# Kernel tuning notes

Hardware: AMD Instinct MI355X
Metric: run time of the kernel (lower is better)

## Reference

```python
import jax, jax.numpy as jnp
import numpy as np

RADIUS = 0.2
NSAMPLE = 32


def ball_query(new_xyz, xyz, radius, nsample):
    # new_xyz: (B, M, 3), xyz: (B, N, 3) -> idx: (B, M, nsample) int32
    B, M, _ = new_xyz.shape
    N = xyz.shape[1]
    # pairwise squared distances (B, M, N)
    diff = new_xyz[:, :, None, :] - xyz[:, None, :, :]
    dist2 = jnp.sum(diff * diff, axis=-1)
    mask = dist2 < (radius * radius)
    ar = jnp.arange(N, dtype=jnp.int32)
    masked = jnp.where(mask, ar[None, None, :], jnp.int32(N + 1))  # (B,M,N)
    sorted_idx = jnp.sort(masked, axis=2)[:, :, :nsample]          # (B,M,nsample)
    invalid = sorted_idx >= N
    first = sorted_idx[:, :, 0:1]
    idx = jnp.where(invalid, jnp.broadcast_to(first, sorted_idx.shape), sorted_idx)
    return idx


def group_points(points, idx):
    # points: (B, C, N), idx: (B, M, nsample) -> (B, C, M, nsample)
    B, C, N = points.shape
    M, ns = idx.shape[1], idx.shape[2]
    flat = jnp.broadcast_to(idx.reshape(B, 1, M * ns), (B, C, M * ns))
    return jnp.take_along_axis(points, flat, axis=2).reshape(B, C, M, ns)


def setup_inputs() -> dict:
    key = jax.random.key(0)
    k1, k2, k3 = jax.random.split(key, 3)
    xyz = jax.random.uniform(k1, (8, 16384, 3), dtype=jnp.float32)
    new_xyz = jax.random.uniform(k2, (8, 1024, 3), dtype=jnp.float32)
    features = jax.random.normal(k3, (8, 64, 16384), dtype=jnp.float32)
    return {"xyz": xyz, "new_xyz": new_xyz, "features": features}


def reference(xyz, new_xyz, features):
    idx = ball_query(new_xyz, xyz, RADIUS, NSAMPLE)          # (B,M,ns)
    xyz_t = jnp.transpose(xyz, (0, 2, 1))                    # (B,3,N)
    grouped_xyz = group_points(xyz_t, idx)                   # (B,3,M,ns)
    grouped_xyz = grouped_xyz - jnp.transpose(new_xyz, (0, 2, 1))[:, :, :, None]
    grouped_features = group_points(features, idx)           # (B,C,M,ns)
    new_features = jnp.concatenate([grouped_xyz, grouped_features], axis=1)
    return new_features                                      # (B, 3+C, M, ns)
```

## Files before the change

### kernel.cpp

```cpp
#include <hip/hip_runtime.h>


#define N_PTS   16384
#define M_Q     1024
#define B_SZ    8
#define NSAMP   32
#define NCH     64
#define R2      0.04f
#define OUT_CH  (3 + NCH)

typedef float f4 __attribute__((ext_vector_type(4)));

__global__ __launch_bounds__(256) void transpose_kernel(
    const float* __restrict__ feat, float* __restrict__ ft)
{
    __shared__ float tile[64][65];
    const int b   = blockIdx.x & 7;
    const int n0  = (blockIdx.x >> 3) << 6;
    const int tid = threadIdx.x;
    const float* __restrict__ fb = feat + (size_t)b * NCH * N_PTS;
    float* __restrict__ tb       = ft   + ((size_t)b * N_PTS + n0) * NCH;

#pragma unroll
    for (int j = 0; j < 16; ++j) {
        const int idx = j * 256 + tid;
        const int c = idx >> 6, nn = idx & 63;
        tile[c][nn] = __builtin_nontemporal_load(&fb[(size_t)c * N_PTS + n0 + nn]);
    }
    __syncthreads();
    const int c4 = tid & 15;
    const int r  = tid >> 4;
#pragma unroll
    for (int j = 0; j < 4; ++j) {
        const int nn = j * 16 + r;
        f4 o;
        o.x = tile[c4 * 4 + 0][nn];
        o.y = tile[c4 * 4 + 1][nn];
        o.z = tile[c4 * 4 + 2][nn];
        o.w = tile[c4 * 4 + 3][nn];
        *(f4*)(&tb[(size_t)nn * NCH + c4 * 4]) = o;
    }
}

__global__ __launch_bounds__(256) void qg_main(
    const float* __restrict__ xyz,
    const float* __restrict__ new_xyz,
    const float* __restrict__ ft,
    float* __restrict__ out)
{
    const int tid  = threadIdx.x;
    const int w    = tid >> 6;
    const int lane = tid & 63;
    const int b    = blockIdx.x & 7;
    const int m    = ((blockIdx.x >> 3) << 2) + w;
    const int q    = (b << 10) + m;

    __shared__ float pxyz[4][NSAMP][4];
    __shared__ float tile[4][32][33];

    const float cx = new_xyz[q * 3 + 0];
    const float cy = new_xyz[q * 3 + 1];
    const float cz = new_xyz[q * 3 + 2];
    const float* __restrict__ xb = xyz + (size_t)b * N_PTS * 3;

    const unsigned long long lmask = (1ull << lane) - 1ull;
    int cnt = 0;
    float Ax = xb[lane * 3 + 0],        Ay = xb[lane * 3 + 1],        Az = xb[lane * 3 + 2];
    float Bx = xb[(64 + lane) * 3 + 0], By = xb[(64 + lane) * 3 + 1], Bz = xb[(64 + lane) * 3 + 2];

    for (int base = 0; ; base += 128) {
        const int  nbase = base + 128;
        const bool more  = nbase < N_PTS;
        const int  pA = more ? nbase + lane : lane;
        const int  pB = pA + 64;
        const float nAx = xb[pA * 3 + 0], nAy = xb[pA * 3 + 1], nAz = xb[pA * 3 + 2];
        const float nBx = xb[pB * 3 + 0], nBy = xb[pB * 3 + 1], nBz = xb[pB * 3 + 2];

        {
            const float dx = __fsub_rn(cx, Ax), dy = __fsub_rn(cy, Ay), dz = __fsub_rn(cz, Az);
            const float d2 = __fadd_rn(__fadd_rn(__fmul_rn(dx, dx), __fmul_rn(dy, dy)),
                                       __fmul_rn(dz, dz));
            const bool hit = d2 < R2;
            const unsigned long long mk = __ballot(hit);
            if (hit) {
                const int slot = cnt + __popcll(mk & lmask);
                if (slot < NSAMP) {
                    pxyz[w][slot][0] = Ax;
                    pxyz[w][slot][1] = Ay;
                    pxyz[w][slot][2] = Az;
                    pxyz[w][slot][3] = __int_as_float(base + lane);
                }
            }
            cnt += (int)__popcll(mk);
        }
        {
            const float dx = __fsub_rn(cx, Bx), dy = __fsub_rn(cy, By), dz = __fsub_rn(cz, Bz);
            const float d2 = __fadd_rn(__fadd_rn(__fmul_rn(dx, dx), __fmul_rn(dy, dy)),
                                       __fmul_rn(dz, dz));
            const bool hit = d2 < R2;
            const unsigned long long mk = __ballot(hit);
            if (hit) {
                const int slot = cnt + __popcll(mk & lmask);
                if (slot < NSAMP) {
                    pxyz[w][slot][0] = Bx;
                    pxyz[w][slot][1] = By;
                    pxyz[w][slot][2] = Bz;
                    pxyz[w][slot][3] = __int_as_float(base + 64 + lane);
                }
            }
            cnt += (int)__popcll(mk);
        }
        if (cnt >= NSAMP || !more) break;
        Ax = nAx; Ay = nAy; Az = nAz;
        Bx = nBx; By = nBy; Bz = nBz;
    }

    if (lane < NSAMP && cnt < NSAMP) {
        float v0x, v0y, v0z, v0w;
        if (cnt > 0) {
            v0x = pxyz[w][0][0]; v0y = pxyz[w][0][1];
            v0z = pxyz[w][0][2]; v0w = pxyz[w][0][3];
        } else {
            v0x = xb[0]; v0y = xb[1]; v0z = xb[2]; v0w = __int_as_float(0);
        }
        if (lane >= cnt) {
            pxyz[w][lane][0] = v0x; pxyz[w][lane][1] = v0y;
            pxyz[w][lane][2] = v0z; pxyz[w][lane][3] = v0w;
        }
    }

    float* __restrict__ ob = out + ((size_t)b * OUT_CH * M_Q + (size_t)m) * NSAMP;

    if (lane < 24) {
        const int c  = lane >> 3;
        const int s4 = lane & 7;
        const float ctr = (c == 0) ? cx : ((c == 1) ? cy : cz);
        f4 o;
        o.x = __fsub_rn(pxyz[w][s4 * 4 + 0][c], ctr);
        o.y = __fsub_rn(pxyz[w][s4 * 4 + 1][c], ctr);
        o.z = __fsub_rn(pxyz[w][s4 * 4 + 2][c], ctr);
        o.w = __fsub_rn(pxyz[w][s4 * 4 + 3][c], ctr);
        __builtin_nontemporal_store(o, (f4*)&ob[(size_t)c * (M_Q * NSAMP) + s4 * 4]);
    }

    const float* __restrict__ ftb = ft + (size_t)b * N_PTS * NCH;
    const int sgrp = lane >> 3;
    const int c4   = lane & 7;

#pragma unroll
    for (int chunk = 0; chunk < 2; ++chunk) {
        f4 vals[4];
#pragma unroll
        for (int i = 0; i < 4; ++i) {
            const int s = i * 8 + sgrp;
            const int n = __float_as_int(pxyz[w][s][3]);
            vals[i] = *(const f4*)(ftb + (size_t)n * NCH + chunk * 32 + c4 * 4);
        }
#pragma unroll
        for (int i = 0; i < 4; ++i) {
            const int s = i * 8 + sgrp;
            tile[w][c4 * 4 + 0][s] = vals[i].x;
            tile[w][c4 * 4 + 1][s] = vals[i].y;
            tile[w][c4 * 4 + 2][s] = vals[i].z;
            tile[w][c4 * 4 + 3][s] = vals[i].w;
        }
#pragma unroll
        for (int j = 0; j < 4; ++j) {
            const int c_loc = j * 8 + (lane >> 3);
            const int s4    = lane & 7;
            f4 o;
            o.x = tile[w][c_loc][s4 * 4 + 0];
            o.y = tile[w][c_loc][s4 * 4 + 1];
            o.z = tile[w][c_loc][s4 * 4 + 2];
            o.w = tile[w][c_loc][s4 * 4 + 3];
            __builtin_nontemporal_store(
                o, (f4*)&ob[(size_t)(3 + chunk * 32 + c_loc) * (M_Q * NSAMP) + s4 * 4]);
        }
    }
}

__global__ __launch_bounds__(256) void qg_fallback(
    const float* __restrict__ xyz, const float* __restrict__ new_xyz,
    const float* __restrict__ feat, float* __restrict__ out)
{
    const int tid  = threadIdx.x;
    const int w    = tid >> 6;
    const int lane = tid & 63;
    const int q    = blockIdx.x * 4 + w;
    const int b    = q >> 10;
    const int m    = q & (M_Q - 1);

    __shared__ int idx_sh[4][NSAMP];

    const float cx = new_xyz[q * 3 + 0];
    const float cy = new_xyz[q * 3 + 1];
    const float cz = new_xyz[q * 3 + 2];
    const float* __restrict__ xb = xyz + (size_t)b * N_PTS * 3;

    int cnt = 0;
    for (int base = 0; base < N_PTS && cnt < NSAMP; base += 64) {
        const int n = base + lane;
        const float dx = __fsub_rn(cx, xb[n * 3 + 0]);
        const float dy = __fsub_rn(cy, xb[n * 3 + 1]);
        const float dz = __fsub_rn(cz, xb[n * 3 + 2]);
        const float d2 = __fadd_rn(__fadd_rn(__fmul_rn(dx, dx), __fmul_rn(dy, dy)),
                                   __fmul_rn(dz, dz));
        const bool hit = d2 < R2;
        const unsigned long long mk = __ballot(hit);
        if (hit) {
            const int slot = cnt + __popcll(mk & ((1ull << lane) - 1ull));
            if (slot < NSAMP) idx_sh[w][slot] = n;
        }
        cnt += (int)__popcll(mk);
    }
    __syncthreads();
    if (lane < NSAMP) {
        const int v0 = (cnt > 0) ? idx_sh[w][0] : 0;
        if (lane >= cnt) idx_sh[w][lane] = v0;
    }
    __syncthreads();

    const float* __restrict__ fb = feat + (size_t)b * NCH * N_PTS;
    float* __restrict__ ob = out + ((size_t)b * OUT_CH * M_Q + (size_t)m) * NSAMP;
    for (int e = lane; e < OUT_CH * NSAMP; e += 64) {
        const int c = e >> 5, s = e & 31;
        const int n = idx_sh[w][s];
        float v;
        if (c < 3) {
            const float ctr = (c == 0) ? cx : ((c == 1) ? cy : cz);
            v = __fsub_rn(xb[n * 3 + c], ctr);
        } else {
            v = fb[(size_t)(c - 3) * N_PTS + n];
        }
        ob[(size_t)c * (M_Q * NSAMP) + s] = v;
    }
}

extern "C" void kernel_launch(void* const* d_in, const int* in_sizes, int n_in,
                              void* d_out, int out_size, void* d_ws, size_t ws_size,
                              hipStream_t stream) {
    const float* xyz     = (const float*)d_in[0];
    const float* new_xyz = (const float*)d_in[1];
    const float* feat    = (const float*)d_in[2];
    float* out           = (float*)d_out;

    const size_t need = (size_t)B_SZ * N_PTS * NCH * sizeof(float);
    if (ws_size >= need) {
        transpose_kernel<<<B_SZ * (N_PTS / 64), 256, 0, stream>>>(feat, (float*)d_ws);
        qg_main<<<(B_SZ * M_Q) / 4, 256, 0, stream>>>(xyz, new_xyz, (const float*)d_ws, out);
    } else {
        qg_fallback<<<(B_SZ * M_Q) / 4, 256, 0, stream>>>(xyz, new_xyz, feat, out);
    }
}
```

Measured before the change: 143.4 us.

## Split ball query into fused transpose kernel with SoA xyz and separate grouping

A new pass converts xyz to structure-of-arrays so the ball-query scan can use vectorized f4 loads over 256 points per iteration. The ball query now runs in the same launch as the feature transpose, with interleaved block types, so the latency-bound search overlaps the bandwidth-bound transpose. Relative offsets and indices are written to a workspace meta buffer that a separate group kernel reads. This adds a kernel launch and extra workspace traffic, and the scan drops the software prefetch of the next chunk.

Measured after the change: 125.9 us. -12.2%, faster.

```diff
diff --git a/kernel.cpp b/kernel.cpp
--- a/kernel.cpp
+++ b/kernel.cpp
@@ -11,40 +11,137 @@
 
 typedef float f4 __attribute__((ext_vector_type(4)));
 
-__global__ __launch_bounds__(256) void transpose_kernel(
-    const float* __restrict__ feat, float* __restrict__ ft)
+__global__ __launch_bounds__(256) void soa_kernel(
+    const float* __restrict__ xyz,
+    float* __restrict__ xs, float* __restrict__ ys, float* __restrict__ zs)
+{
+    const int i = blockIdx.x * 256 + threadIdx.x;
+    const float* src = xyz + (size_t)i * 3;
+    xs[i] = src[0];
+    ys[i] = src[1];
+    zs[i] = src[2];
+}
+
+__global__ __launch_bounds__(256) void fat_kernel(
+    const float* __restrict__ feat,
+    const float* __restrict__ new_xyz,
+    const float* __restrict__ xs, const float* __restrict__ ys,
+    const float* __restrict__ zs,
+    float* __restrict__ ft,
+    f4* __restrict__ meta)
 {
     __shared__ float tile[64][65];
-    const int b   = blockIdx.x & 7;
-    const int n0  = (blockIdx.x >> 3) << 6;
-    const int tid = threadIdx.x;
-    const float* __restrict__ fb = feat + (size_t)b * NCH * N_PTS;
-    float* __restrict__ tb       = ft   + ((size_t)b * N_PTS + n0) * NCH;
-
-#pragma unroll
-    for (int j = 0; j < 16; ++j) {
-        const int idx = j * 256 + tid;
-        const int c = idx >> 6, nn = idx & 63;
-        tile[c][nn] = __builtin_nontemporal_load(&fb[(size_t)c * N_PTS + n0 + nn]);
-    }
-    __syncthreads();
-    const int c4 = tid & 15;
-    const int r  = tid >> 4;
-#pragma unroll
-    for (int j = 0; j < 4; ++j) {
-        const int nn = j * 16 + r;
-        f4 o;
-        o.x = tile[c4 * 4 + 0][nn];
-        o.y = tile[c4 * 4 + 1][nn];
-        o.z = tile[c4 * 4 + 2][nn];
-        o.w = tile[c4 * 4 + 3][nn];
-        *(f4*)(&tb[(size_t)nn * NCH + c4 * 4]) = o;
-    }
-}
-
-__global__ __launch_bounds__(256) void qg_main(
-    const float* __restrict__ xyz,
-    const float* __restrict__ new_xyz,
+    __shared__ float pxyz[4][NSAMP][4];
+    const int tid  = threadIdx.x;
+    const int u    = (blockIdx.x & 7) | ((blockIdx.x >> 4) << 3);
+    const int type = (blockIdx.x >> 3) & 1;
+    const int b    = u & 7;
+
+    if (type == 0) {
+        const int n0 = (u >> 3) << 6;
+        const float* __restrict__ fb = feat + (size_t)b * NCH * N_PTS;
+        float* __restrict__ tb       = ft   + ((size_t)b * N_PTS + n0) * NCH;
+#pragma unroll
+        for (int j = 0; j < 16; ++j) {
+            const int idx = j * 256 + tid;
+            const int c = idx >> 6, nn = idx & 63;
+            tile[c][nn] = __builtin_nontemporal_load(&fb[(size_t)c * N_PTS + n0 + nn]);
+        }
+        __syncthreads();
+        const int c4 = tid & 15;
+        const int r  = tid >> 4;
+#pragma unroll
+        for (int j = 0; j < 4; ++j) {
+            const int nn = j * 16 + r;
+            f4 o;
+            o.x = tile[c4 * 4 + 0][nn];
+            o.y = tile[c4 * 4 + 1][nn];
+            o.z = tile[c4 * 4 + 2][nn];
+            o.w = tile[c4 * 4 + 3][nn];
+            *(f4*)(&tb[(size_t)nn * NCH + c4 * 4]) = o;
+        }
+        return;
+    }
+
+    const int w    = tid >> 6;
+    const int lane = tid & 63;
+    const int m    = ((u >> 3) << 2) + w;
+    const int q    = (b << 10) + m;
+
+    const float cx = new_xyz[q * 3 + 0];
+    const float cy = new_xyz[q * 3 + 1];
+    const float cz = new_xyz[q * 3 + 2];
+    const float* __restrict__ xsb = xs + (size_t)b * N_PTS;
+    const float* __restrict__ ysb = ys + (size_t)b * N_PTS;
+    const float* __restrict__ zsb = zs + (size_t)b * N_PTS;
+
+    const unsigned long long lt = (1ull << lane) - 1ull;
+    int cnt = 0;
+    for (int base = 0; base < N_PTS; base += 256) {
+        const int p0 = base + 4 * lane;
+        const f4 X = *(const f4*)(xsb + p0);
+        const f4 Y = *(const f4*)(ysb + p0);
+        const f4 Z = *(const f4*)(zsb + p0);
+        float dxs[4], dys[4], dzs[4];
+        unsigned long long bl[4];
+        bool hits[4];
+#pragma unroll
+        for (int j = 0; j < 4; ++j) {
+            const float dx = __fsub_rn(cx, X[j]);
+            const float dy = __fsub_rn(cy, Y[j]);
+            const float dz = __fsub_rn(cz, Z[j]);
+            const float d2 = __fadd_rn(__fadd_rn(__fmul_rn(dx, dx), __fmul_rn(dy, dy)),
+                                       __fmul_rn(dz, dz));
+            dxs[j] = dx; dys[j] = dy; dzs[j] = dz;
+            hits[j] = d2 < R2;
+            bl[j]   = __ballot(hits[j]);
+        }
+        const int pre = __popcll(bl[0] & lt) + __popcll(bl[1] & lt)
+                      + __popcll(bl[2] & lt) + __popcll(bl[3] & lt);
+        int own = 0;
+#pragma unroll
+        for (int j = 0; j < 4; ++j) {
+            if (hits[j]) {
+                const int slot = cnt + pre + own;
+                if (slot < NSAMP) {
+                    pxyz[w][slot][0] = -dxs[j];
+                    pxyz[w][slot][1] = -dys[j];
+                    pxyz[w][slot][2] = -dzs[j];
+                    pxyz[w][slot][3] = __int_as_float(p0 + j);
+                }
+            }
+            own += (int)((bl[j] >> lane) & 1ull);
+        }
+        cnt += __popcll(bl[0]) + __popcll(bl[1]) + __popcll(bl[2]) + __popcll(bl[3]);
+        if (cnt >= NSAMP) break;
+    }
+
+    if (lane < NSAMP && cnt < NSAMP) {
+        float v0x, v0y, v0z, v0w;
+        if (cnt > 0) {
+            v0x = pxyz[w][0][0]; v0y = pxyz[w][0][1];
+            v0z = pxyz[w][0][2]; v0w = pxyz[w][0][3];
+        } else {
+            v0x = __fsub_rn(xsb[0], cx); v0y = __fsub_rn(ysb[0], cy);
+            v0z = __fsub_rn(zsb[0], cz); v0w = __int_as_float(0);
+        }
+        if (lane >= cnt) {
+            pxyz[w][lane][0] = v0x; pxyz[w][lane][1] = v0y;
+            pxyz[w][lane][2] = v0z; pxyz[w][lane][3] = v0w;
+        }
+    }
+    if (lane < NSAMP) {
+        f4 mv;
+        mv.x = pxyz[w][lane][0];
+        mv.y = pxyz[w][lane][1];
+        mv.z = pxyz[w][lane][2];
+        mv.w = pxyz[w][lane][3];
+        meta[(size_t)q * NSAMP + lane] = mv;
+    }
+}
+
+__global__ __launch_bounds__(256) void group_kernel(
+    const f4* __restrict__ meta,
     const float* __restrict__ ft,
     float* __restrict__ out)
 {
@@ -58,75 +155,12 @@
     __shared__ float pxyz[4][NSAMP][4];
     __shared__ float tile[4][32][33];
 
-    const float cx = new_xyz[q * 3 + 0];
-    const float cy = new_xyz[q * 3 + 1];
-    const float cz = new_xyz[q * 3 + 2];
-    const float* __restrict__ xb = xyz + (size_t)b * N_PTS * 3;
-
-    const unsigned long long lmask = (1ull << lane) - 1ull;
-    int cnt = 0;
-    float Ax = xb[lane * 3 + 0],        Ay = xb[lane * 3 + 1],        Az = xb[lane * 3 + 2];
-    float Bx = xb[(64 + lane) * 3 + 0], By = xb[(64 + lane) * 3 + 1], Bz = xb[(64 + lane) * 3 + 2];
-
-    for (int base = 0; ; base += 128) {
-        const int  nbase = base + 128;
-        const bool more  = nbase < N_PTS;
-        const int  pA = more ? nbase + lane : lane;
-        const int  pB = pA + 64;
-        const float nAx = xb[pA * 3 + 0], nAy = xb[pA * 3 + 1], nAz = xb[pA * 3 + 2];
-        const float nBx = xb[pB * 3 + 0], nBy = xb[pB * 3 + 1], nBz = xb[pB * 3 + 2];
-
-        {
-            const float dx = __fsub_rn(cx, Ax), dy = __fsub_rn(cy, Ay), dz = __fsub_rn(cz, Az);
-            const float d2 = __fadd_rn(__fadd_rn(__fmul_rn(dx, dx), __fmul_rn(dy, dy)),
-                                       __fmul_rn(dz, dz));
-            const bool hit = d2 < R2;
-            const unsigned long long mk = __ballot(hit);
-            if (hit) {
-                const int slot = cnt + __popcll(mk & lmask);
-                if (slot < NSAMP) {
-                    pxyz[w][slot][0] = Ax;
-                    pxyz[w][slot][1] = Ay;
-                    pxyz[w][slot][2] = Az;
-                    pxyz[w][slot][3] = __int_as_float(base + lane);
-                }
-            }
-            cnt += (int)__popcll(mk);
-        }
-        {
-            const float dx = __fsub_rn(cx, Bx), dy = __fsub_rn(cy, By), dz = __fsub_rn(cz, Bz);
-            const float d2 = __fadd_rn(__fadd_rn(__fmul_rn(dx, dx), __fmul_rn(dy, dy)),
-                                       __fmul_rn(dz, dz));
-            const bool hit = d2 < R2;
-            const unsigned long long mk = __ballot(hit);
-            if (hit) {
-                const int slot = cnt + __popcll(mk & lmask);
-                if (slot < NSAMP) {
-                    pxyz[w][slot][0] = Bx;
-                    pxyz[w][slot][1] = By;
-                    pxyz[w][slot][2] = Bz;
-                    pxyz[w][slot][3] = __int_as_float(base + 64 + lane);
-                }
-            }
-            cnt += (int)__popcll(mk);
-        }
-        if (cnt >= NSAMP || !more) break;
-        Ax = nAx; Ay = nAy; Az = nAz;
-        Bx = nBx; By = nBy; Bz = nBz;
-    }
-
-    if (lane < NSAMP && cnt < NSAMP) {
-        float v0x, v0y, v0z, v0w;
-        if (cnt > 0) {
-            v0x = pxyz[w][0][0]; v0y = pxyz[w][0][1];
-            v0z = pxyz[w][0][2]; v0w = pxyz[w][0][3];
-        } else {
-            v0x = xb[0]; v0y = xb[1]; v0z = xb[2]; v0w = __int_as_float(0);
-        }
-        if (lane >= cnt) {
-            pxyz[w][lane][0] = v0x; pxyz[w][lane][1] = v0y;
-            pxyz[w][lane][2] = v0z; pxyz[w][lane][3] = v0w;
-        }
+    if (lane < NSAMP) {
+        const f4 mv = meta[(size_t)q * NSAMP + lane];
+        pxyz[w][lane][0] = mv.x;
+        pxyz[w][lane][1] = mv.y;
+        pxyz[w][lane][2] = mv.z;
+        pxyz[w][lane][3] = mv.w;
     }
 
     float* __restrict__ ob = out + ((size_t)b * OUT_CH * M_Q + (size_t)m) * NSAMP;
@@ -134,12 +168,11 @@
     if (lane < 24) {
         const int c  = lane >> 3;
         const int s4 = lane & 7;
-        const float ctr = (c == 0) ? cx : ((c == 1) ? cy : cz);
         f4 o;
-        o.x = __fsub_rn(pxyz[w][s4 * 4 + 0][c], ctr);
-        o.y = __fsub_rn(pxyz[w][s4 * 4 + 1][c], ctr);
-        o.z = __fsub_rn(pxyz[w][s4 * 4 + 2][c], ctr);
-        o.w = __fsub_rn(pxyz[w][s4 * 4 + 3][c], ctr);
+        o.x = pxyz[w][s4 * 4 + 0][c];
+        o.y = pxyz[w][s4 * 4 + 1][c];
+        o.z = pxyz[w][s4 * 4 + 2][c];
+        o.w = pxyz[w][s4 * 4 + 3][c];
         __builtin_nontemporal_store(o, (f4*)&ob[(size_t)c * (M_Q * NSAMP) + s4 * 4]);
     }
 
@@ -244,10 +277,21 @@
     const float* feat    = (const float*)d_in[2];
     float* out           = (float*)d_out;
 
-    const size_t need = (size_t)B_SZ * N_PTS * NCH * sizeof(float);
+    const size_t ft_elems   = (size_t)B_SZ * N_PTS * NCH;
+    const size_t soa_elems  = (size_t)B_SZ * N_PTS;
+    const size_t meta_elems = (size_t)B_SZ * M_Q * NSAMP * 4;
+    const size_t need = (ft_elems + 3 * soa_elems + meta_elems) * sizeof(float);
+
+    float* ft   = (float*)d_ws;
+    float* xs   = ft + ft_elems;
+    float* ys   = xs + soa_elems;
+    float* zs   = ys + soa_elems;
+    f4*    meta = (f4*)(zs + soa_elems);
+
     if (ws_size >= need) {
-        transpose_kernel<<<B_SZ * (N_PTS / 64), 256, 0, stream>>>(feat, (float*)d_ws);
-        qg_main<<<(B_SZ * M_Q) / 4, 256, 0, stream>>>(xyz, new_xyz, (const float*)d_ws, out);
+        soa_kernel<<<(B_SZ * N_PTS) / 256, 256, 0, stream>>>(xyz, xs, ys, zs);
+        fat_kernel<<<4096, 256, 0, stream>>>(feat, new_xyz, xs, ys, zs, ft, meta);
+        group_kernel<<<(B_SZ * M_Q) / 4, 256, 0, stream>>>(meta, ft, out);
     } else {
         qg_fallback<<<(B_SZ * M_Q) / 4, 256, 0, stream>>>(xyz, new_xyz, feat, out);
     }
```

## Overlap feature transpose with ball query in a fused kernel, split gathering

Applied to the files above, without the earlier changes.

Restructures the pipeline into three kernels. A pack kernel converts xyz to float4. A combined kernel interleaves feature-transpose blocks with ball-query blocks so the bandwidth-bound transpose and the latency-bound search run concurrently; the query blocks write the relative xyz output and the sample indices to a workspace. A separate gather kernel then reads those indices and gathers the transposed features. This adds one launch, an index round-trip through global memory and extra workspace, in exchange for overlap and vectorized xyz loads.

Result: faster. 127.9 us (-10.9%).

```diff
diff --git a/kernel.cpp b/kernel.cpp
--- a/kernel.cpp
+++ b/kernel.cpp
@@ -11,40 +11,151 @@
 
 typedef float f4 __attribute__((ext_vector_type(4)));
 
-__global__ __launch_bounds__(256) void transpose_kernel(
-    const float* __restrict__ feat, float* __restrict__ ft)
+__global__ __launch_bounds__(256) void pack_kernel(
+    const float* __restrict__ xyz, f4* __restrict__ pk)
+{
+    const int i = blockIdx.x * 256 + threadIdx.x;
+    const float* src = xyz + (size_t)i * 3;
+    f4 v;
+    v.x = src[0]; v.y = src[1]; v.z = src[2]; v.w = 0.0f;
+    pk[i] = v;
+}
+
+__global__ __launch_bounds__(256) void fat_kernel(
+    const float* __restrict__ feat,
+    const float* __restrict__ new_xyz,
+    const f4*    __restrict__ pk,
+    float* __restrict__ ft,
+    int*   __restrict__ meta,
+    float* __restrict__ out)
 {
     __shared__ float tile[64][65];
-    const int b   = blockIdx.x & 7;
-    const int n0  = (blockIdx.x >> 3) << 6;
-    const int tid = threadIdx.x;
-    const float* __restrict__ fb = feat + (size_t)b * NCH * N_PTS;
-    float* __restrict__ tb       = ft   + ((size_t)b * N_PTS + n0) * NCH;
-
-#pragma unroll
-    for (int j = 0; j < 16; ++j) {
-        const int idx = j * 256 + tid;
-        const int c = idx >> 6, nn = idx & 63;
-        tile[c][nn] = __builtin_nontemporal_load(&fb[(size_t)c * N_PTS + n0 + nn]);
-    }
-    __syncthreads();
-    const int c4 = tid & 15;
-    const int r  = tid >> 4;
-#pragma unroll
-    for (int j = 0; j < 4; ++j) {
-        const int nn = j * 16 + r;
+    __shared__ float pxyz[4][NSAMP][4];
+    const int tid  = threadIdx.x;
+    const int u    = (blockIdx.x & 7) | ((blockIdx.x >> 4) << 3);
+    const int type = (blockIdx.x >> 3) & 1;
+    const int b    = u & 7;
+
+    if (type == 0) {
+        const int n0 = (u >> 3) << 6;
+        const float* __restrict__ fb = feat + (size_t)b * NCH * N_PTS;
+        float* __restrict__ tb       = ft   + ((size_t)b * N_PTS + n0) * NCH;
+#pragma unroll
+        for (int j = 0; j < 16; ++j) {
+            const int idx = j * 256 + tid;
+            const int c = idx >> 6, nn = idx & 63;
+            tile[c][nn] = __builtin_nontemporal_load(&fb[(size_t)c * N_PTS + n0 + nn]);
+        }
+        __syncthreads();
+        const int c4 = tid & 15;
+        const int r  = tid >> 4;
+#pragma unroll
+        for (int j = 0; j < 4; ++j) {
+            const int nn = j * 16 + r;
+            f4 o;
+            o.x = tile[c4 * 4 + 0][nn];
+            o.y = tile[c4 * 4 + 1][nn];
+            o.z = tile[c4 * 4 + 2][nn];
+            o.w = tile[c4 * 4 + 3][nn];
+            *(f4*)(&tb[(size_t)nn * NCH + c4 * 4]) = o;
+        }
+        return;
+    }
+
+    const int w    = tid >> 6;
+    const int lane = tid & 63;
+    const int m    = ((u >> 3) << 2) + w;
+    const int q    = (b << 10) + m;
+
+    const float cx = new_xyz[q * 3 + 0];
+    const float cy = new_xyz[q * 3 + 1];
+    const float cz = new_xyz[q * 3 + 2];
+    const f4* __restrict__ pb = pk + (size_t)b * N_PTS;
+
+    const unsigned long long lt = (1ull << lane) - 1ull;
+    int cnt = 0;
+    f4 PA = pb[lane];
+    f4 PB = pb[64 + lane];
+
+    for (int base = 0; ; base += 128) {
+        const int  nbase = base + 128;
+        const bool more  = nbase < N_PTS;
+        const int  pAi = more ? nbase + lane : lane;
+        const f4 nPA = pb[pAi];
+        const f4 nPB = pb[pAi + 64];
+
+        {
+            const float dx = __fsub_rn(cx, PA.x), dy = __fsub_rn(cy, PA.y), dz = __fsub_rn(cz, PA.z);
+            const float d2 = __fadd_rn(__fadd_rn(__fmul_rn(dx, dx), __fmul_rn(dy, dy)),
+                                       __fmul_rn(dz, dz));
+            const bool hit = d2 < R2;
+            const unsigned long long mk = __ballot(hit);
+            if (hit) {
+                const int slot = cnt + __popcll(mk & lt);
+                if (slot < NSAMP) {
+                    pxyz[w][slot][0] = -dx;
+                    pxyz[w][slot][1] = -dy;
+                    pxyz[w][slot][2] = -dz;
+                    pxyz[w][slot][3] = __int_as_float(base + lane);
+                }
+            }
+            cnt += (int)__popcll(mk);
+        }
+        {
+            const float dx = __fsub_rn(cx, PB.x), dy = __fsub_rn(cy, PB.y), dz = __fsub_rn(cz, PB.z);
+            const float d2 = __fadd_rn(__fadd_rn(__fmul_rn(dx, dx), __fmul_rn(dy, dy)),
+                                       __fmul_rn(dz, dz));
+            const bool hit = d2 < R2;
+            const unsigned long long mk = __ballot(hit);
+            if (hit) {
+                const int slot = cnt + __popcll(mk & lt);
+                if (slot < NSAMP) {
+                    pxyz[w][slot][0] = -dx;
+                    pxyz[w][slot][1] = -dy;
+                    pxyz[w][slot][2] = -dz;
+                    pxyz[w][slot][3] = __int_as_float(base + 64 + lane);
+                }
+            }
+            cnt += (int)__popcll(mk);
+        }
+        if (cnt >= NSAMP || !more) break;
+        PA = nPA; PB = nPB;
+    }
+
+    if (lane < NSAMP && cnt < NSAMP) {
+        float v0x, v0y, v0z, v0w;
+        if (cnt > 0) {
+            v0x = pxyz[w][0][0]; v0y = pxyz[w][0][1];
+            v0z = pxyz[w][0][2]; v0w = pxyz[w][0][3];
+        } else {
+            const f4 p0 = pb[0];
+            v0x = __fsub_rn(p0.x, cx); v0y = __fsub_rn(p0.y, cy);
+            v0z = __fsub_rn(p0.z, cz); v0w = __int_as_float(0);
+        }
+        if (lane >= cnt) {
+            pxyz[w][lane][0] = v0x; pxyz[w][lane][1] = v0y;
+            pxyz[w][lane][2] = v0z; pxyz[w][lane][3] = v0w;
+        }
+    }
+
+    float* __restrict__ ob = out + ((size_t)b * OUT_CH * M_Q + (size_t)m) * NSAMP;
+    if (lane < 24) {
+        const int c  = lane >> 3;
+        const int s4 = lane & 7;
         f4 o;
-        o.x = tile[c4 * 4 + 0][nn];
-        o.y = tile[c4 * 4 + 1][nn];
-        o.z = tile[c4 * 4 + 2][nn];
-        o.w = tile[c4 * 4 + 3][nn];
-        *(f4*)(&tb[(size_t)nn * NCH + c4 * 4]) = o;
-    }
-}
-
-__global__ __launch_bounds__(256) void qg_main(
-    const float* __restrict__ xyz,
-    const float* __restrict__ new_xyz,
+        o.x = pxyz[w][s4 * 4 + 0][c];
+        o.y = pxyz[w][s4 * 4 + 1][c];
+        o.z = pxyz[w][s4 * 4 + 2][c];
+        o.w = pxyz[w][s4 * 4 + 3][c];
+        __builtin_nontemporal_store(o, (f4*)&ob[(size_t)c * (M_Q * NSAMP) + s4 * 4]);
+    }
+
+    if (lane < NSAMP)
+        meta[(size_t)q * NSAMP + lane] = __float_as_int(pxyz[w][lane][3]);
+}
+
+__global__ __launch_bounds__(256) void group_kernel(
+    const int*   __restrict__ meta,
     const float* __restrict__ ft,
     float* __restrict__ out)
 {
@@ -55,94 +166,13 @@
     const int m    = ((blockIdx.x >> 3) << 2) + w;
     const int q    = (b << 10) + m;
 
-    __shared__ float pxyz[4][NSAMP][4];
+    __shared__ int   ishare[4][NSAMP];
     __shared__ float tile[4][32][33];
 
-    const float cx = new_xyz[q * 3 + 0];
-    const float cy = new_xyz[q * 3 + 1];
-    const float cz = new_xyz[q * 3 + 2];
-    const float* __restrict__ xb = xyz + (size_t)b * N_PTS * 3;
-
-    const unsigned long long lmask = (1ull << lane) - 1ull;
-    int cnt = 0;
-    float Ax = xb[lane * 3 + 0],        Ay = xb[lane * 3 + 1],        Az = xb[lane * 3 + 2];
-    float Bx = xb[(64 + lane) * 3 + 0], By = xb[(64 + lane) * 3 + 1], Bz = xb[(64 + lane) * 3 + 2];
-
-    for (int base = 0; ; base += 128) {
-        const int  nbase = base + 128;
-        const bool more  = nbase < N_PTS;
-        const int  pA = more ? nbase + lane : lane;
-        const int  pB = pA + 64;
-        const float nAx = xb[pA * 3 + 0], nAy = xb[pA * 3 + 1], nAz = xb[pA * 3 + 2];
-        const float nBx = xb[pB * 3 + 0], nBy = xb[pB * 3 + 1], nBz = xb[pB * 3 + 2];
-
-        {
-            const float dx = __fsub_rn(cx, Ax), dy = __fsub_rn(cy, Ay), dz = __fsub_rn(cz, Az);
-            const float d2 = __fadd_rn(__fadd_rn(__fmul_rn(dx, dx), __fmul_rn(dy, dy)),
-                                       __fmul_rn(dz, dz));
-            const bool hit = d2 < R2;
-            const unsigned long long mk = __ballot(hit);
-            if (hit) {
-                const int slot = cnt + __popcll(mk & lmask);
-                if (slot < NSAMP) {
-                    pxyz[w][slot][0] = Ax;
-                    pxyz[w][slot][1] = Ay;
-                    pxyz[w][slot][2] = Az;
-                    pxyz[w][slot][3] = __int_as_float(base + lane);
-                }
-            }
-            cnt += (int)__popcll(mk);
-        }
-        {
-            const float dx = __fsub_rn(cx, Bx), dy = __fsub_rn(cy, By), dz = __fsub_rn(cz, Bz);
-            const float d2 = __fadd_rn(__fadd_rn(__fmul_rn(dx, dx), __fmul_rn(dy, dy)),
-                                       __fmul_rn(dz, dz));
-            const bool hit = d2 < R2;
-            const unsigned long long mk = __ballot(hit);
-            if (hit) {
-                const int slot = cnt + __popcll(mk & lmask);
-                if (slot < NSAMP) {
-                    pxyz[w][slot][0] = Bx;
-                    pxyz[w][slot][1] = By;
-                    pxyz[w][slot][2] = Bz;
-                    pxyz[w][slot][3] = __int_as_float(base + 64 + lane);
-                }
-            }
-            cnt += (int)__popcll(mk);
-        }
-        if (cnt >= NSAMP || !more) break;
-        Ax = nAx; Ay = nAy; Az = nAz;
-        Bx = nBx; By = nBy; Bz = nBz;
-    }
-
-    if (lane < NSAMP && cnt < NSAMP) {
-        float v0x, v0y, v0z, v0w;
-        if (cnt > 0) {
-            v0x = pxyz[w][0][0]; v0y = pxyz[w][0][1];
-            v0z = pxyz[w][0][2]; v0w = pxyz[w][0][3];
-        } else {
-            v0x = xb[0]; v0y = xb[1]; v0z = xb[2]; v0w = __int_as_float(0);
-        }
-        if (lane >= cnt) {
-            pxyz[w][lane][0] = v0x; pxyz[w][lane][1] = v0y;
-            pxyz[w][lane][2] = v0z; pxyz[w][lane][3] = v0w;
-        }
-    }
+    if (lane < NSAMP)
+        ishare[w][lane] = meta[(size_t)q * NSAMP + lane];
 
     float* __restrict__ ob = out + ((size_t)b * OUT_CH * M_Q + (size_t)m) * NSAMP;
-
-    if (lane < 24) {
-        const int c  = lane >> 3;
-        const int s4 = lane & 7;
-        const float ctr = (c == 0) ? cx : ((c == 1) ? cy : cz);
-        f4 o;
-        o.x = __fsub_rn(pxyz[w][s4 * 4 + 0][c], ctr);
-        o.y = __fsub_rn(pxyz[w][s4 * 4 + 1][c], ctr);
-        o.z = __fsub_rn(pxyz[w][s4 * 4 + 2][c], ctr);
-        o.w = __fsub_rn(pxyz[w][s4 * 4 + 3][c], ctr);
-        __builtin_nontemporal_store(o, (f4*)&ob[(size_t)c * (M_Q * NSAMP) + s4 * 4]);
-    }
-
     const float* __restrict__ ftb = ft + (size_t)b * N_PTS * NCH;
     const int sgrp = lane >> 3;
     const int c4   = lane & 7;
@@ -153,7 +183,7 @@
 #pragma unroll
         for (int i = 0; i < 4; ++i) {
             const int s = i * 8 + sgrp;
-            const int n = __float_as_int(pxyz[w][s][3]);
+            const int n = ishare[w][s];
             vals[i] = *(const f4*)(ftb + (size_t)n * NCH + chunk * 32 + c4 * 4);
         }
 #pragma unroll
@@ -244,10 +274,20 @@
     const float* feat    = (const float*)d_in[2];
     float* out           = (float*)d_out;
 
-    const size_t need = (size_t)B_SZ * N_PTS * NCH * sizeof(float);
+    const size_t ft_elems   = (size_t)B_SZ * N_PTS * NCH;
+    const size_t pk_elems   = (size_t)B_SZ * N_PTS;
+    const size_t meta_elems = (size_t)B_SZ * M_Q * NSAMP;
+    const size_t need = ft_elems * sizeof(float) + pk_elems * sizeof(f4)
+                      + meta_elems * sizeof(int);
+
+    float* ft   = (float*)d_ws;
+    f4*    pk   = (f4*)(ft + ft_elems);
+    int*   meta = (int*)(pk + pk_elems);
+
     if (ws_size >= need) {
-        transpose_kernel<<<B_SZ * (N_PTS / 64), 256, 0, stream>>>(feat, (float*)d_ws);
-        qg_main<<<(B_SZ * M_Q) / 4, 256, 0, stream>>>(xyz, new_xyz, (const float*)d_ws, out);
+        pack_kernel<<<(B_SZ * N_PTS) / 256, 256, 0, stream>>>(xyz, pk);
+        fat_kernel<<<4096, 256, 0, stream>>>(feat, new_xyz, pk, ft, meta, out);
+        group_kernel<<<(B_SZ * M_Q) / 4, 256, 0, stream>>>(meta, ft, out);
     } else {
         qg_fallback<<<(B_SZ * M_Q) / 4, 256, 0, stream>>>(xyz, new_xyz, feat, out);
     }
```

## Share SoA point chunks across block waves via double-buffered LDS scan

Applied to the files above, without the earlier changes.

Adds a pre-pass that splits xyz into separate x, y and z arrays. The ball-query scan now has all four waves of a block load 256-point chunks of those arrays into double-buffered shared memory cooperatively, so every wave reuses the same loads instead of each wave fetching strided AoS data on its own. The kernel keeps the relative offsets from the distance computation in shared memory, which removes the later subtraction. The cost is a __syncthreads per chunk, with all waves held until the last one finishes, plus an extra kernel launch and more workspace.

After: 129.6 us. 9.7% less time.

```diff
diff --git a/kernel.cpp b/kernel.cpp
--- a/kernel.cpp
+++ b/kernel.cpp
@@ -8,8 +8,20 @@
 #define NCH     64
 #define R2      0.04f
 #define OUT_CH  (3 + NCH)
+#define CHUNK   256
 
 typedef float f4 __attribute__((ext_vector_type(4)));
+
+__global__ __launch_bounds__(256) void soa_kernel(
+    const float* __restrict__ xyz,
+    float* __restrict__ xs, float* __restrict__ ys, float* __restrict__ zs)
+{
+    const int i = blockIdx.x * 256 + threadIdx.x;
+    const float* src = xyz + (size_t)i * 3;
+    xs[i] = src[0];
+    ys[i] = src[1];
+    zs[i] = src[2];
+}
 
 __global__ __launch_bounds__(256) void transpose_kernel(
     const float* __restrict__ feat, float* __restrict__ ft)
@@ -43,9 +55,10 @@
 }
 
 __global__ __launch_bounds__(256) void qg_main(
-    const float* __restrict__ xyz,
     const float* __restrict__ new_xyz,
     const float* __restrict__ ft,
+    const float* __restrict__ xs, const float* __restrict__ ys,
+    const float* __restrict__ zs,
     float* __restrict__ out)
 {
     const int tid  = threadIdx.x;
@@ -55,64 +68,77 @@
     const int m    = ((blockIdx.x >> 3) << 2) + w;
     const int q    = (b << 10) + m;
 
+    __shared__ float xbuf[2][CHUNK], ybuf[2][CHUNK], zbuf[2][CHUNK];
     __shared__ float pxyz[4][NSAMP][4];
     __shared__ float tile[4][32][33];
+    __shared__ int   donef[4];
 
     const float cx = new_xyz[q * 3 + 0];
     const float cy = new_xyz[q * 3 + 1];
     const float cz = new_xyz[q * 3 + 2];
-    const float* __restrict__ xb = xyz + (size_t)b * N_PTS * 3;
-
-    const unsigned long long lmask = (1ull << lane) - 1ull;
-    int cnt = 0;
-    float Ax = xb[lane * 3 + 0],        Ay = xb[lane * 3 + 1],        Az = xb[lane * 3 + 2];
-    float Bx = xb[(64 + lane) * 3 + 0], By = xb[(64 + lane) * 3 + 1], Bz = xb[(64 + lane) * 3 + 2];
-
-    for (int base = 0; ; base += 128) {
-        const int  nbase = base + 128;
-        const bool more  = nbase < N_PTS;
-        const int  pA = more ? nbase + lane : lane;
-        const int  pB = pA + 64;
-        const float nAx = xb[pA * 3 + 0], nAy = xb[pA * 3 + 1], nAz = xb[pA * 3 + 2];
-        const float nBx = xb[pB * 3 + 0], nBy = xb[pB * 3 + 1], nBz = xb[pB * 3 + 2];
-
-        {
-            const float dx = __fsub_rn(cx, Ax), dy = __fsub_rn(cy, Ay), dz = __fsub_rn(cz, Az);
-            const float d2 = __fadd_rn(__fadd_rn(__fmul_rn(dx, dx), __fmul_rn(dy, dy)),
-                                       __fmul_rn(dz, dz));
-            const bool hit = d2 < R2;
-            const unsigned long long mk = __ballot(hit);
-            if (hit) {
-                const int slot = cnt + __popcll(mk & lmask);
-                if (slot < NSAMP) {
-                    pxyz[w][slot][0] = Ax;
-                    pxyz[w][slot][1] = Ay;
-                    pxyz[w][slot][2] = Az;
-                    pxyz[w][slot][3] = __int_as_float(base + lane);
+    const float* __restrict__ xsb = xs + (size_t)b * N_PTS;
+    const float* __restrict__ ysb = ys + (size_t)b * N_PTS;
+    const float* __restrict__ zsb = zs + (size_t)b * N_PTS;
+
+    const unsigned long long lt = (1ull << lane) - 1ull;
+    int  cnt    = 0;
+    bool mydone = false;
+
+    xbuf[0][tid] = xsb[tid];
+    ybuf[0][tid] = ysb[tid];
+    zbuf[0][tid] = zsb[tid];
+    if (tid < 4) donef[tid] = 0;
+    __syncthreads();
+
+    for (int i = 0; ; ++i) {
+        const int base      = i * CHUNK;
+        const int base_next = base + CHUNK;
+        const bool more     = base_next < N_PTS;
+        float nx = 0.f, ny = 0.f, nz = 0.f;
+        if (more) {
+            nx = xsb[base_next + tid];
+            ny = ysb[base_next + tid];
+            nz = zsb[base_next + tid];
+        }
+
+        if (!mydone) {
+            const int cur = i & 1;
+#pragma unroll
+            for (int s = 0; s < 4; ++s) {
+                const int  o  = s * 64 + lane;
+                const float px = xbuf[cur][o];
+                const float py = ybuf[cur][o];
+                const float pz = zbuf[cur][o];
+                const float dx = __fsub_rn(cx, px);
+                const float dy = __fsub_rn(cy, py);
+                const float dz = __fsub_rn(cz, pz);
+                const float d2 = __fadd_rn(__fadd_rn(__fmul_rn(dx, dx), __fmul_rn(dy, dy)),
+                                           __fmul_rn(dz, dz));
+                const bool hit = d2 < R2;
+                const unsigned long long mk = __ballot(hit);
+                if (hit) {
+                    const int slot = cnt + __popcll(mk & lt);
+                    if (slot < NSAMP) {
+                        pxyz[w][slot][0] = -dx;
+                        pxyz[w][slot][1] = -dy;
+                        pxyz[w][slot][2] = -dz;
+                        pxyz[w][slot][3] = __int_as_float(base + o);
+                    }
                 }
+                cnt += (int)__popcll(mk);
             }
-            cnt += (int)__popcll(mk);
-        }
-        {
-            const float dx = __fsub_rn(cx, Bx), dy = __fsub_rn(cy, By), dz = __fsub_rn(cz, Bz);
-            const float d2 = __fadd_rn(__fadd_rn(__fmul_rn(dx, dx), __fmul_rn(dy, dy)),
-                                       __fmul_rn(dz, dz));
-            const bool hit = d2 < R2;
-            const unsigned long long mk = __ballot(hit);
-            if (hit) {
-                const int slot = cnt + __popcll(mk & lmask);
-                if (slot < NSAMP) {
-                    pxyz[w][slot][0] = Bx;
-                    pxyz[w][slot][1] = By;
-                    pxyz[w][slot][2] = Bz;
-                    pxyz[w][slot][3] = __int_as_float(base + 64 + lane);
-                }
-            }
-            cnt += (int)__popcll(mk);
-        }
-        if (cnt >= NSAMP || !more) break;
-        Ax = nAx; Ay = nAy; Az = nAz;
-        Bx = nBx; By = nBy; Bz = nBz;
+            mydone = (cnt >= NSAMP);
+            if (lane == 0) donef[w] = mydone ? 1 : 0;
+        }
+
+        if (more) {
+            const int nxt = (i + 1) & 1;
+            xbuf[nxt][tid] = nx;
+            ybuf[nxt][tid] = ny;
+            zbuf[nxt][tid] = nz;
+        }
+        __syncthreads();
+        if (!more || (donef[0] & donef[1] & donef[2] & donef[3])) break;
     }
 
     if (lane < NSAMP && cnt < NSAMP) {
@@ -121,7 +147,8 @@
             v0x = pxyz[w][0][0]; v0y = pxyz[w][0][1];
             v0z = pxyz[w][0][2]; v0w = pxyz[w][0][3];
         } else {
-            v0x = xb[0]; v0y = xb[1]; v0z = xb[2]; v0w = __int_as_float(0);
+            v0x = __fsub_rn(xsb[0], cx); v0y = __fsub_rn(ysb[0], cy);
+            v0z = __fsub_rn(zsb[0], cz); v0w = __int_as_float(0);
         }
         if (lane >= cnt) {
             pxyz[w][lane][0] = v0x; pxyz[w][lane][1] = v0y;
@@ -134,12 +161,11 @@
     if (lane < 24) {
         const int c  = lane >> 3;
         const int s4 = lane & 7;
-        const float ctr = (c == 0) ? cx : ((c == 1) ? cy : cz);
         f4 o;
-        o.x = __fsub_rn(pxyz[w][s4 * 4 + 0][c], ctr);
-        o.y = __fsub_rn(pxyz[w][s4 * 4 + 1][c], ctr);
-        o.z = __fsub_rn(pxyz[w][s4 * 4 + 2][c], ctr);
-        o.w = __fsub_rn(pxyz[w][s4 * 4 + 3][c], ctr);
+        o.x = pxyz[w][s4 * 4 + 0][c];
+        o.y = pxyz[w][s4 * 4 + 1][c];
+        o.z = pxyz[w][s4 * 4 + 2][c];
+        o.w = pxyz[w][s4 * 4 + 3][c];
         __builtin_nontemporal_store(o, (f4*)&ob[(size_t)c * (M_Q * NSAMP) + s4 * 4]);
     }
 
@@ -244,10 +270,19 @@
     const float* feat    = (const float*)d_in[2];
     float* out           = (float*)d_out;
 
-    const size_t need = (size_t)B_SZ * N_PTS * NCH * sizeof(float);
+    const size_t ft_elems  = (size_t)B_SZ * N_PTS * NCH;
+    const size_t soa_elems = (size_t)B_SZ * N_PTS;
+    const size_t need = (ft_elems + 3 * soa_elems) * sizeof(float);
+
+    float* ft = (float*)d_ws;
+    float* xs = ft + ft_elems;
+    float* ys = xs + soa_elems;
+    float* zs = ys + soa_elems;
+
     if (ws_size >= need) {
-        transpose_kernel<<<B_SZ * (N_PTS / 64), 256, 0, stream>>>(feat, (float*)d_ws);
-        qg_main<<<(B_SZ * M_Q) / 4, 256, 0, stream>>>(xyz, new_xyz, (const float*)d_ws, out);
+        soa_kernel<<<(B_SZ * N_PTS) / 256, 256, 0, stream>>>(xyz, xs, ys, zs);
+        transpose_kernel<<<B_SZ * (N_PTS / 64), 256, 0, stream>>>(feat, ft);
+        qg_main<<<(B_SZ * M_Q) / 4, 256, 0, stream>>>(new_xyz, ft, xs, ys, zs, out);
     } else {
         qg_fallback<<<(B_SZ * M_Q) / 4, 256, 0, stream>>>(xyz, new_xyz, feat, out);
     }
```
